# Kernel optimization log

Measured on AMD Instinct MI355X. Metric: run time of the kernel, lower is better.

Reference implementation:

```python
import jax, jax.numpy as jnp
import numpy as np


def setup_inputs() -> dict:
    key = jax.random.key(0)
    ks = jax.random.split(key, 6)
    B, T, S, E, D = 8, 128, 512, 512, 512  # batch, trg_len, src_len, enc_dim, trg_dim
    W_SCALE = 0.03  # small init to keep tanh unsaturated
    return {
        "hidden": jax.random.normal(ks[0], (B, T, D), jnp.float32),
        "encoder_outputs": jax.random.normal(ks[1], (B, S, E), jnp.float32),
        "encoder_mask": jnp.ones((B, S), jnp.float32),
        "W_attn": jax.random.normal(ks[2], (D, E + D), jnp.float32) * W_SCALE,
        "b_attn": jnp.zeros((D,), jnp.float32),
        "W_v": jax.random.normal(ks[3], (1, D), jnp.float32) * W_SCALE,
        "b_v": jnp.zeros((1,), jnp.float32),
        "W_out": jax.random.normal(ks[4], (D, E + D), jnp.float32) * W_SCALE,
    }


def masked_softmax(x, m, axis=-1):
    # faithful to repo: x*m, stable exp, e*m, normalize with eps
    x = x * m
    e_x = jnp.exp(x - jnp.max(x, axis=axis, keepdims=True))
    e_x = e_x * m
    return e_x / (jnp.sum(e_x, axis=axis, keepdims=True) + 1e-6)


def reference(hidden, encoder_outputs, encoder_mask, W_attn, b_attn, W_v, b_v, W_out):
    B, T, D = hidden.shape
    S = encoder_outputs.shape[1]
    # concat order in get_energy is (hidden_i, encoder_outputs), so split W_attn
    W_h = W_attn[:, :D]   # (D_out, trg_dim)
    W_e = W_attn[:, D:]   # (D_out, enc_dim)
    # Linear(concat) == h@W_h^T + e@W_e^T + b; vectorized over all (t, s) pairs
    hp = jnp.einsum('btd,kd->btk', hidden, W_h)            # (B,T,K)
    ep = jnp.einsum('bse,ke->bsk', encoder_outputs, W_e)   # (B,S,K)
    feat = jnp.tanh(hp[:, :, None, :] + ep[:, None, :, :] + b_attn)  # (B,T,S,K)
    energies = jnp.einsum('btsk,k->bts', feat, W_v[0]) + b_v[0]      # (B,T,S)
    # forward: energies * mask, then masked softmax
    m = encoder_mask[:, None, :]  # (B,1,S)
    energies = energies * m
    attn_weights = masked_softmax(energies, m, axis=-1)    # (B,T,S)
    weighted_context = jnp.einsum('bts,bse->bte', attn_weights, encoder_outputs)
    h_cat = jnp.concatenate([weighted_context, hidden], axis=-1)  # (B,T,E+D)
    h_tilde = jnp.tanh(jnp.einsum('btc,dc->btd', h_cat, W_out))   # (B,T,D)
    return h_tilde, weighted_context, attn_weights
```

## Files before the change

### kernel.cpp

```cpp
#include <hip/hip_runtime.h>
#include <hip/hip_bf16.h>
#include <math.h>

typedef unsigned short u16;
typedef unsigned int u32;
typedef __bf16 bf16x8 __attribute__((ext_vector_type(8)));
typedef float f32x4 __attribute__((ext_vector_type(4)));

#define OUT_WC   524288LL
#define OUT_ATTN 1048576LL
#define C2 2.8853900817779268f
#define LOG2E 1.4426950408889634f
#define LAS 40
#define LAS2 72

__device__ inline u16 f2b(float f) {
    return (u16)((__float_as_uint(f) + 0x8000u) >> 16);
}
__device__ inline float b2f(u16 v) { return __uint_as_float(((u32)v) << 16); }
__device__ inline u32 pkcvt(float x, float y) {
    __hip_bfloat162 h = __float22bfloat162_rn(make_float2(x, y));
    return *(u32*)&h;
}
__device__ inline float tanh_fast(float x) {
    return 1.f - 2.f * __builtin_amdgcn_rcpf(__builtin_amdgcn_exp2f(C2 * x) + 1.f);
}

__global__ __launch_bounds__(256) void proj(
    const float* __restrict__ hidden, const float* __restrict__ enc,
    const float* __restrict__ Wattn, const float* __restrict__ battn,
    const float* __restrict__ Wout,
    float* __restrict__ hp, u16* __restrict__ ept, float* __restrict__ hh,
    u16* __restrict__ enc_bf)
{
    __shared__ u16 lA[64 * LAS2];
    __shared__ u16 lB[64 * LAS2];
    const int tid = threadIdx.x;
    const int wvi = tid >> 6, ln = tid & 63;
    const int wm = wvi >> 1, wn = wvi & 1;
    const int l16 = ln & 15, quad = ln >> 4;
    const int blk = blockIdx.x;
    int bx, by, zz = 0, lda, ldb, mode;
    const float *A, *B;
    if (blk < 512) {
        mode = 0;
        zz = blk >> 6; by = (blk >> 3) & 7; bx = blk & 7;
        A = Wattn + 512; lda = 1024;
        B = enc + (long long)zz * 262144; ldb = 512;
    } else if (blk < 640) {
        mode = 1;
        int i = blk - 512; by = i >> 3; bx = i & 7;
        A = hidden; lda = 512;
        B = Wattn; ldb = 1024;
    } else {
        mode = 2;
        int i = blk - 640; by = i >> 3; bx = i & 7;
        A = hidden; lda = 512;
        B = Wout + 512; ldb = 1024;
    }
    const int m0 = by * 64, n0 = bx * 64;
    const int srow = tid >> 2, scol = (tid & 3) * 16;
    const float* Ap = A + (long long)(m0 + srow) * lda + scol;
    const float* Bp = B + (long long)(n0 + srow) * ldb + scol;
    const bool wr_enc = (mode == 0) && (by == 0);

    f32x4 acc00 = {0,0,0,0}, acc01 = {0,0,0,0}, acc10 = {0,0,0,0}, acc11 = {0,0,0,0};

    float4 pa0, pa1, pa2, pa3, pb0, pb1, pb2, pb3;
    #define PROJ_LOADK(k0) do { \
        pa0 = *(const float4*)(Ap + (k0));      pa1 = *(const float4*)(Ap + (k0) + 4);  \
        pa2 = *(const float4*)(Ap + (k0) + 8);  pa3 = *(const float4*)(Ap + (k0) + 12); \
        pb0 = *(const float4*)(Bp + (k0));      pb1 = *(const float4*)(Bp + (k0) + 4);  \
        pb2 = *(const float4*)(Bp + (k0) + 8);  pb3 = *(const float4*)(Bp + (k0) + 12); } while (0)

    PROJ_LOADK(0);
    for (int step = 0; step < 8; ++step) {
        uint4 av0 = make_uint4(pkcvt(pa0.x, pa0.y), pkcvt(pa0.z, pa0.w),
                               pkcvt(pa1.x, pa1.y), pkcvt(pa1.z, pa1.w));
        uint4 av1 = make_uint4(pkcvt(pa2.x, pa2.y), pkcvt(pa2.z, pa2.w),
                               pkcvt(pa3.x, pa3.y), pkcvt(pa3.z, pa3.w));
        uint4 bv0 = make_uint4(pkcvt(pb0.x, pb0.y), pkcvt(pb0.z, pb0.w),
                               pkcvt(pb1.x, pb1.y), pkcvt(pb1.z, pb1.w));
        uint4 bv1 = make_uint4(pkcvt(pb2.x, pb2.y), pkcvt(pb2.z, pb2.w),
                               pkcvt(pb3.x, pb3.y), pkcvt(pb3.z, pb3.w));
        if (wr_enc) {
            u16* ed = enc_bf + (long long)zz * 262144 +
                      (long long)(n0 + srow) * 512 + step * 64 + scol;
            *(uint4*)ed = bv0;
            *(uint4*)(ed + 8) = bv1;
        }
        __syncthreads();
        *(uint4*)&lA[srow * LAS2 + scol]     = av0;
        *(uint4*)&lA[srow * LAS2 + scol + 8] = av1;
        *(uint4*)&lB[srow * LAS2 + scol]     = bv0;
        *(uint4*)&lB[srow * LAS2 + scol + 8] = bv1;
        __syncthreads();
        if (step < 7) PROJ_LOADK((step + 1) * 64);
        #pragma unroll
        for (int kh = 0; kh < 2; ++kh) {
            bf16x8 a0 = *(const bf16x8*)&lA[(wm * 32      + l16) * LAS2 + kh * 32 + quad * 8];
            bf16x8 a1 = *(const bf16x8*)&lA[(wm * 32 + 16 + l16) * LAS2 + kh * 32 + quad * 8];
            bf16x8 b0 = *(const bf16x8*)&lB[(wn * 32      + l16) * LAS2 + kh * 32 + quad * 8];
            bf16x8 b1 = *(const bf16x8*)&lB[(wn * 32 + 16 + l16) * LAS2 + kh * 32 + quad * 8];
            acc00 = __builtin_amdgcn_mfma_f32_16x16x32_bf16(a0, b0, acc00, 0, 0, 0);
            acc01 = __builtin_amdgcn_mfma_f32_16x16x32_bf16(a0, b1, acc01, 0, 0, 0);
            acc10 = __builtin_amdgcn_mfma_f32_16x16x32_bf16(a1, b0, acc10, 0, 0, 0);
            acc11 = __builtin_amdgcn_mfma_f32_16x16x32_bf16(a1, b1, acc11, 0, 0, 0);
        }
    }
    #undef PROJ_LOADK

    const f32x4* accs[4] = { &acc00, &acc01, &acc10, &acc11 };
    #pragma unroll
    for (int i = 0; i < 2; ++i) {
        #pragma unroll
        for (int j = 0; j < 2; ++j) {
            const f32x4& a = *accs[i * 2 + j];
            #pragma unroll
            for (int r = 0; r < 4; ++r) {
                int m = m0 + wm * 32 + i * 16 + quad * 4 + r;
                int n = n0 + wn * 32 + j * 16 + l16;
                float v = a[r];
                if (mode == 0)
                    ept[(long long)zz * 262144 + (long long)m * 512 + n] =
                        f2b(__builtin_amdgcn_exp2f(C2 * v));
                else if (mode == 1)
                    hp[(long long)m * 512 + n] = C2 * (v + battn[n]);
                else
                    hh[(long long)m * 512 + n] = v;
            }
        }
    }
}

__device__ inline float wred_sum(float v) {
    #pragma unroll
    for (int i = 32; i > 0; i >>= 1) v += __shfl_xor(v, i);
    return v;
}
__device__ inline float wred_max(float v) {
    #pragma unroll
    for (int i = 32; i > 0; i >>= 1) v = fmaxf(v, __shfl_xor(v, i));
    return v;
}

__device__ inline void proc8(uint4 c, float4 hw, float* a0, float* a1) {
    u32 cc[4] = {c.x, c.y, c.z, c.w};
    #pragma unroll
    for (int i = 0; i < 4; ++i) {
        float xl = __uint_as_float(cc[i] << 16);
        float xh = __uint_as_float(cc[i] & 0xFFFF0000u);
        float rl0 = __builtin_amdgcn_rcpf(fmaf(hw.x, xl, 1.f));
        float rh0 = __builtin_amdgcn_rcpf(fmaf(hw.x, xh, 1.f));
        float rl1 = __builtin_amdgcn_rcpf(fmaf(hw.y, xl, 1.f));
        float rh1 = __builtin_amdgcn_rcpf(fmaf(hw.y, xh, 1.f));
        a0[2*i]   = fmaf(hw.z, rl0, a0[2*i]);
        a0[2*i+1] = fmaf(hw.z, rh0, a0[2*i+1]);
        a1[2*i]   = fmaf(hw.z, rl1, a1[2*i]);
        a1[2*i+1] = fmaf(hw.z, rh1, a1[2*i+1]);
    }
}
__device__ inline void wcproc2(uint4 c, float2 ap, float* acc0, float* acc1) {
    u32 cc[4] = {c.x, c.y, c.z, c.w};
    #pragma unroll
    for (int i = 0; i < 4; ++i) {
        float el = __uint_as_float(cc[i] << 16);
        float eh = __uint_as_float(cc[i] & 0xFFFF0000u);
        acc0[2*i]   = fmaf(ap.x, el, acc0[2*i]);
        acc0[2*i+1] = fmaf(ap.x, eh, acc0[2*i+1]);
        acc1[2*i]   = fmaf(ap.y, el, acc1[2*i]);
        acc1[2*i+1] = fmaf(ap.y, eh, acc1[2*i+1]);
    }
}

__global__ __launch_bounds__(1024) void energies(
    const float* __restrict__ maskp, const float* __restrict__ hp,
    const u16* __restrict__ ept, const float* __restrict__ Wv,
    const float* __restrict__ bvp, const u16* __restrict__ enc_bf,
    float* __restrict__ attn, float* __restrict__ wc)
{
    __shared__ __align__(16) float4 hpw[512];
    __shared__ float pa[2][16][512];
    __shared__ float aL[512][2];
    __shared__ float red[16];
    const int tid = threadIdx.x;
    const int b  = blockIdx.x & 7;
    const int t0 = (blockIdx.x >> 3) * 2;
    const int th = tid >> 9;
    const int k5 = tid & 511;
    const long long row0 = (long long)(b * 128 + t0) * 512;

    float hv = hp[row0 + (long long)th * 512 + k5];
    float eh = __builtin_amdgcn_exp2f(hv);
    float* hpwf = (float*)hpw;
    hpwf[k5 * 4 + th] = eh;
    float w = 0.f;
    if (th == 0) { w = Wv[k5]; hpwf[k5 * 4 + 2] = w; }
    float wsum = wred_sum(w);
    if ((tid & 63) == 0) red[tid >> 6] = wsum;
    __syncthreads();
    float sumWv = 0.f;
    #pragma unroll
    for (int i = 0; i < 16; ++i) sumWv += red[i];

    const int kg = tid >> 6, sl = tid & 63;
    const int s0 = sl * 8;
    const u16* eb = ept + (long long)b * 262144 + (kg * 32) * 512 + s0;
    const float4* hq = &hpw[kg * 32];

    float a0[8] = {0,0,0,0,0,0,0,0}, a1[8] = {0,0,0,0,0,0,0,0};
    uint4 c0 = *(const uint4*)(eb);
    uint4 c1 = *(const uint4*)(eb + 512);
    for (int kk = 0; kk < 30; kk += 2) {
        const u16* nb = eb + (kk + 2) * 512;
        uint4 n0 = *(const uint4*)(nb);
        uint4 n1 = *(const uint4*)(nb + 512);
        proc8(c0, hq[kk],     a0, a1);
        proc8(c1, hq[kk + 1], a0, a1);
        c0 = n0; c1 = n1;
    }
    proc8(c0, hq[30], a0, a1);
    proc8(c1, hq[31], a0, a1);

    *(float4*)&pa[0][kg][s0]     = make_float4(a0[0], a0[1], a0[2], a0[3]);
    *(float4*)&pa[0][kg][s0 + 4] = make_float4(a0[4], a0[5], a0[6], a0[7]);
    *(float4*)&pa[1][kg][s0]     = make_float4(a1[0], a1[1], a1[2], a1[3]);
    *(float4*)&pa[1][kg][s0 + 4] = make_float4(a1[4], a1[5], a1[6], a1[7]);
    __syncthreads();

    float A = 0.f;
    #pragma unroll
    for (int g = 0; g < 16; ++g) A += pa[th][g][k5];
    float mv = maskp[(long long)b * 512 + k5];
    float bv0 = bvp[0];
    float r = (bv0 + sumWv - 2.f * A) * mv; r *= mv;

    float vmax = wred_max(r);
    if ((tid & 63) == 0) red[tid >> 6] = vmax;
    __syncthreads();
    float mx = red[th * 8];
    #pragma unroll
    for (int i = 1; i < 8; ++i) mx = fmaxf(mx, red[th * 8 + i]);

    float ex = __builtin_amdgcn_exp2f((r - mx) * LOG2E) * mv;
    float vsum = wred_sum(ex);
    __syncthreads();
    if ((tid & 63) == 0) red[tid >> 6] = vsum;
    __syncthreads();
    float sm = 0.f;
    #pragma unroll
    for (int i = 0; i < 8; ++i) sm += red[th * 8 + i];
    float at = ex * (1.f / (sm + 1e-6f));
    attn[row0 + (long long)th * 512 + k5] = at;
    aL[k5][th] = at;
    __syncthreads();

    const int eg = tid & 63, sg = tid >> 6;
    const u16* encb = enc_bf + (long long)b * 262144 + (long long)(sg * 32) * 512 + eg * 8;
    const float2* aq = (const float2*)&aL[sg * 32][0];
    float acc0[8] = {0,0,0,0,0,0,0,0}, acc1[8] = {0,0,0,0,0,0,0,0};
    uint4 e0 = *(const uint4*)(encb);
    uint4 e1 = *(const uint4*)(encb + 512);
    for (int j = 0; j < 30; j += 2) {
        uint4 f0 = *(const uint4*)(encb + (long long)(j + 2) * 512);
        uint4 f1 = *(const uint4*)(encb + (long long)(j + 3) * 512);
        wcproc2(e0, aq[j],     acc0, acc1);
        wcproc2(e1, aq[j + 1], acc0, acc1);
        e0 = f0; e1 = f1;
    }
    wcproc2(e0, aq[30], acc0, acc1);
    wcproc2(e1, aq[31], acc0, acc1);

    *(float4*)&pa[0][sg][eg * 8]     = make_float4(acc0[0], acc0[1], acc0[2], acc0[3]);
    *(float4*)&pa[0][sg][eg * 8 + 4] = make_float4(acc0[4], acc0[5], acc0[6], acc0[7]);
    *(float4*)&pa[1][sg][eg * 8]     = make_float4(acc1[0], acc1[1], acc1[2], acc1[3]);
    *(float4*)&pa[1][sg][eg * 8 + 4] = make_float4(acc1[4], acc1[5], acc1[6], acc1[7]);
    __syncthreads();

    float wcv = 0.f;
    #pragma unroll
    for (int g = 0; g < 16; ++g) wcv += pa[th][g][k5];
    wc[row0 + (long long)th * 512 + k5] = wcv;
}

__global__ __launch_bounds__(256) void hout_k(
    const float* __restrict__ wc, const float* __restrict__ Wout,
    float* __restrict__ out)
{
    __shared__ u16 lA[32 * LAS];
    __shared__ u16 lB[64 * LAS];
    const int tid = threadIdx.x;
    const int wvi = tid >> 6, ln = tid & 63;
    const int l16 = ln & 15, quad = ln >> 4;
    const int msub = wvi & 1, npair = wvi >> 1;
    const int m0 = blockIdx.y * 32, n0 = blockIdx.x * 64;
    const int rowA = tid >> 3, kofA = (tid & 7) * 4;
    const int rowB = tid >> 2, kofB = (tid & 3) * 8;
    const float* Apw = wc + (long long)(m0 + rowA) * 512 + kofA;
    const float* Bpw = Wout + (long long)(n0 + rowB) * 1024 + kofB;
    f32x4 acc0 = {0,0,0,0}, acc1 = {0,0,0,0};

    float4 av, bw0, bw1;
    av  = *(const float4*)(Apw);
    bw0 = *(const float4*)(Bpw);
    bw1 = *(const float4*)(Bpw + 4);
    for (int k0 = 0; k0 < 512; k0 += 32) {
        uint2 aw = make_uint2(pkcvt(av.x, av.y), pkcvt(av.z, av.w));
        uint4 bv = make_uint4(pkcvt(bw0.x, bw0.y), pkcvt(bw0.z, bw0.w),
                              pkcvt(bw1.x, bw1.y), pkcvt(bw1.z, bw1.w));
        __syncthreads();
        *(uint2*)&lA[rowA * LAS + kofA] = aw;
        int kk = kofB ^ (((rowB >> 3) & 3) << 3);
        *(uint4*)&lB[rowB * LAS + kk] = bv;
        __syncthreads();
        if (k0 < 480) {
            av  = *(const float4*)(Apw + k0 + 32);
            bw0 = *(const float4*)(Bpw + k0 + 32);
            bw1 = *(const float4*)(Bpw + k0 + 36);
        }
        bf16x8 a = *(const bf16x8*)&lA[(msub * 16 + l16) * LAS + quad * 8];
        int nr0 = npair * 32 + l16, nr1 = nr0 + 16;
        bf16x8 b0 = *(const bf16x8*)&lB[nr0 * LAS + (quad * 8 ^ (((nr0 >> 3) & 3) << 3))];
        bf16x8 b1 = *(const bf16x8*)&lB[nr1 * LAS + (quad * 8 ^ (((nr1 >> 3) & 3) << 3))];
        acc0 = __builtin_amdgcn_mfma_f32_16x16x32_bf16(a, b0, acc0, 0, 0, 0);
        acc1 = __builtin_amdgcn_mfma_f32_16x16x32_bf16(a, b1, acc1, 0, 0, 0);
    }
    #pragma unroll
    for (int j = 0; j < 2; ++j) {
        const f32x4& a = j ? acc1 : acc0;
        #pragma unroll
        for (int r = 0; r < 4; ++r) {
            int m = m0 + msub * 16 + quad * 4 + r;
            int n = n0 + npair * 32 + j * 16 + l16;
            long long idx = (long long)m * 512 + n;
            out[idx] = tanh_fast(a[r] + out[idx]);
        }
    }
}

extern "C" void kernel_launch(void* const* d_in, const int* in_sizes, int n_in,
                              void* d_out, int out_size, void* d_ws, size_t ws_size,
                              hipStream_t stream)
{
    const float* hidden = (const float*)d_in[0];
    const float* enc    = (const float*)d_in[1];
    const float* mask   = (const float*)d_in[2];
    const float* Wattn  = (const float*)d_in[3];
    const float* battn  = (const float*)d_in[4];
    const float* Wv     = (const float*)d_in[5];
    const float* bvp    = (const float*)d_in[6];
    const float* Wout   = (const float*)d_in[7];
    float* out = (float*)d_out;

    float* hp     = (float*)d_ws;
    u16*   ept    = (u16*)((char*)d_ws + (2 << 20));
    u16*   enc_bf = (u16*)((char*)d_ws + (6 << 20));

    proj<<<768, 256, 0, stream>>>(hidden, enc, Wattn, battn, Wout,
                                  hp, ept, out , enc_bf);
    energies<<<512, 1024, 0, stream>>>(mask, hp, ept, Wv, bvp, enc_bf,
                                       out + OUT_ATTN, out + OUT_WC);
    hout_k<<<dim3(8, 32, 1), 256, 0, stream>>>(out + OUT_WC, Wout, out);
}
```

Baseline: 150.8 us.

## Fuse three kernels into one cooperative persistent kernel with grid syncs

Replaces the three separate launches (projection GEMMs, energies/softmax/context, output GEMM) with one cooperative kernel of 256 blocks of 1024 threads. Stages are separated by grid.sync. GEMM work is redistributed as 64x64 tasks handled by 16 waves, each computing one 16x16 tile, and each block processes two query-row pairs in the attention stage. This removes launch gaps and inter-kernel drains, at the cost of grid-wide barriers, lower occupancy (one block per CU), smaller per-wave MFMA work, and only half the blocks active in the final GEMM. It falls back to the old three-kernel path if the cooperative launch fails.

Result: slower. 501.1 us (+232.2%).

```diff
diff --git a/kernel.cpp b/kernel.cpp
--- a/kernel.cpp
+++ b/kernel.cpp
@@ -1,6 +1,9 @@
 #include <hip/hip_runtime.h>
 #include <hip/hip_bf16.h>
+#include <hip/hip_cooperative_groups.h>
 #include <math.h>
+
+namespace cg = cooperative_groups;
 
 typedef unsigned short u16;
 typedef unsigned int u32;
@@ -17,13 +20,50 @@
 __device__ inline u16 f2b(float f) {
     return (u16)((__float_as_uint(f) + 0x8000u) >> 16);
 }
-__device__ inline float b2f(u16 v) { return __uint_as_float(((u32)v) << 16); }
 __device__ inline u32 pkcvt(float x, float y) {
     __hip_bfloat162 h = __float22bfloat162_rn(make_float2(x, y));
     return *(u32*)&h;
 }
 __device__ inline float tanh_fast(float x) {
     return 1.f - 2.f * __builtin_amdgcn_rcpf(__builtin_amdgcn_exp2f(C2 * x) + 1.f);
+}
+__device__ inline float wred_sum(float v) {
+    #pragma unroll
+    for (int i = 32; i > 0; i >>= 1) v += __shfl_xor(v, i);
+    return v;
+}
+__device__ inline float wred_max(float v) {
+    #pragma unroll
+    for (int i = 32; i > 0; i >>= 1) v = fmaxf(v, __shfl_xor(v, i));
+    return v;
+}
+__device__ inline void proc8(uint4 c, float4 hw, float* a0, float* a1) {
+    u32 cc[4] = {c.x, c.y, c.z, c.w};
+    #pragma unroll
+    for (int i = 0; i < 4; ++i) {
+        float xl = __uint_as_float(cc[i] << 16);
+        float xh = __uint_as_float(cc[i] & 0xFFFF0000u);
+        float rl0 = __builtin_amdgcn_rcpf(fmaf(hw.x, xl, 1.f));
+        float rh0 = __builtin_amdgcn_rcpf(fmaf(hw.x, xh, 1.f));
+        float rl1 = __builtin_amdgcn_rcpf(fmaf(hw.y, xl, 1.f));
+        float rh1 = __builtin_amdgcn_rcpf(fmaf(hw.y, xh, 1.f));
+        a0[2*i]   = fmaf(hw.z, rl0, a0[2*i]);
+        a0[2*i+1] = fmaf(hw.z, rh0, a0[2*i+1]);
+        a1[2*i]   = fmaf(hw.z, rl1, a1[2*i]);
+        a1[2*i+1] = fmaf(hw.z, rh1, a1[2*i+1]);
+    }
+}
+__device__ inline void wcproc2(uint4 c, float2 ap, float* q0, float* q1) {
+    u32 cc[4] = {c.x, c.y, c.z, c.w};
+    #pragma unroll
+    for (int i = 0; i < 4; ++i) {
+        float el = __uint_as_float(cc[i] << 16);
+        float eh = __uint_as_float(cc[i] & 0xFFFF0000u);
+        q0[2*i]   = fmaf(ap.x, el, q0[2*i]);
+        q0[2*i+1] = fmaf(ap.x, eh, q0[2*i+1]);
+        q1[2*i]   = fmaf(ap.y, el, q1[2*i]);
+        q1[2*i+1] = fmaf(ap.y, eh, q1[2*i+1]);
+    }
 }
 
 __global__ __launch_bounds__(256) void proj(
@@ -43,20 +83,15 @@
     int bx, by, zz = 0, lda, ldb, mode;
     const float *A, *B;
     if (blk < 512) {
-        mode = 0;
-        zz = blk >> 6; by = (blk >> 3) & 7; bx = blk & 7;
+        mode = 0; zz = blk >> 6; by = (blk >> 3) & 7; bx = blk & 7;
         A = Wattn + 512; lda = 1024;
         B = enc + (long long)zz * 262144; ldb = 512;
     } else if (blk < 640) {
-        mode = 1;
-        int i = blk - 512; by = i >> 3; bx = i & 7;
-        A = hidden; lda = 512;
-        B = Wattn; ldb = 1024;
+        mode = 1; int i = blk - 512; by = i >> 3; bx = i & 7;
+        A = hidden; lda = 512; B = Wattn; ldb = 1024;
     } else {
-        mode = 2;
-        int i = blk - 640; by = i >> 3; bx = i & 7;
-        A = hidden; lda = 512;
-        B = Wout + 512; ldb = 1024;
+        mode = 2; int i = blk - 640; by = i >> 3; bx = i & 7;
+        A = hidden; lda = 512; B = Wout + 512; ldb = 1024;
     }
     const int m0 = by * 64, n0 = bx * 64;
     const int srow = tid >> 2, scol = (tid & 3) * 16;
@@ -65,14 +100,12 @@
     const bool wr_enc = (mode == 0) && (by == 0);
 
     f32x4 acc00 = {0,0,0,0}, acc01 = {0,0,0,0}, acc10 = {0,0,0,0}, acc11 = {0,0,0,0};
-
     float4 pa0, pa1, pa2, pa3, pb0, pb1, pb2, pb3;
     #define PROJ_LOADK(k0) do { \
         pa0 = *(const float4*)(Ap + (k0));      pa1 = *(const float4*)(Ap + (k0) + 4);  \
         pa2 = *(const float4*)(Ap + (k0) + 8);  pa3 = *(const float4*)(Ap + (k0) + 12); \
         pb0 = *(const float4*)(Bp + (k0));      pb1 = *(const float4*)(Bp + (k0) + 4);  \
         pb2 = *(const float4*)(Bp + (k0) + 8);  pb3 = *(const float4*)(Bp + (k0) + 12); } while (0)
-
     PROJ_LOADK(0);
     for (int step = 0; step < 8; ++step) {
         uint4 av0 = make_uint4(pkcvt(pa0.x, pa0.y), pkcvt(pa0.z, pa0.w),
@@ -109,7 +142,6 @@
         }
     }
     #undef PROJ_LOADK
-
     const f32x4* accs[4] = { &acc00, &acc01, &acc10, &acc11 };
     #pragma unroll
     for (int i = 0; i < 2; ++i) {
@@ -133,46 +165,6 @@
     }
 }
 
-__device__ inline float wred_sum(float v) {
-    #pragma unroll
-    for (int i = 32; i > 0; i >>= 1) v += __shfl_xor(v, i);
-    return v;
-}
-__device__ inline float wred_max(float v) {
-    #pragma unroll
-    for (int i = 32; i > 0; i >>= 1) v = fmaxf(v, __shfl_xor(v, i));
-    return v;
-}
-
-__device__ inline void proc8(uint4 c, float4 hw, float* a0, float* a1) {
-    u32 cc[4] = {c.x, c.y, c.z, c.w};
-    #pragma unroll
-    for (int i = 0; i < 4; ++i) {
-        float xl = __uint_as_float(cc[i] << 16);
-        float xh = __uint_as_float(cc[i] & 0xFFFF0000u);
-        float rl0 = __builtin_amdgcn_rcpf(fmaf(hw.x, xl, 1.f));
-        float rh0 = __builtin_amdgcn_rcpf(fmaf(hw.x, xh, 1.f));
-        float rl1 = __builtin_amdgcn_rcpf(fmaf(hw.y, xl, 1.f));
-        float rh1 = __builtin_amdgcn_rcpf(fmaf(hw.y, xh, 1.f));
-        a0[2*i]   = fmaf(hw.z, rl0, a0[2*i]);
-        a0[2*i+1] = fmaf(hw.z, rh0, a0[2*i+1]);
-        a1[2*i]   = fmaf(hw.z, rl1, a1[2*i]);
-        a1[2*i+1] = fmaf(hw.z, rh1, a1[2*i+1]);
-    }
-}
-__device__ inline void wcproc2(uint4 c, float2 ap, float* acc0, float* acc1) {
-    u32 cc[4] = {c.x, c.y, c.z, c.w};
-    #pragma unroll
-    for (int i = 0; i < 4; ++i) {
-        float el = __uint_as_float(cc[i] << 16);
-        float eh = __uint_as_float(cc[i] & 0xFFFF0000u);
-        acc0[2*i]   = fmaf(ap.x, el, acc0[2*i]);
-        acc0[2*i+1] = fmaf(ap.x, eh, acc0[2*i+1]);
-        acc1[2*i]   = fmaf(ap.y, el, acc1[2*i]);
-        acc1[2*i+1] = fmaf(ap.y, eh, acc1[2*i+1]);
-    }
-}
-
 __global__ __launch_bounds__(1024) void energies(
     const float* __restrict__ maskp, const float* __restrict__ hp,
     const u16* __restrict__ ept, const float* __restrict__ Wv,
@@ -258,23 +250,23 @@
     const int eg = tid & 63, sg = tid >> 6;
     const u16* encb = enc_bf + (long long)b * 262144 + (long long)(sg * 32) * 512 + eg * 8;
     const float2* aq = (const float2*)&aL[sg * 32][0];
-    float acc0[8] = {0,0,0,0,0,0,0,0}, acc1[8] = {0,0,0,0,0,0,0,0};
+    float q0[8] = {0,0,0,0,0,0,0,0}, q1[8] = {0,0,0,0,0,0,0,0};
     uint4 e0 = *(const uint4*)(encb);
     uint4 e1 = *(const uint4*)(encb + 512);
     for (int j = 0; j < 30; j += 2) {
         uint4 f0 = *(const uint4*)(encb + (long long)(j + 2) * 512);
         uint4 f1 = *(const uint4*)(encb + (long long)(j + 3) * 512);
-        wcproc2(e0, aq[j],     acc0, acc1);
-        wcproc2(e1, aq[j + 1], acc0, acc1);
+        wcproc2(e0, aq[j],     q0, q1);
+        wcproc2(e1, aq[j + 1], q0, q1);
         e0 = f0; e1 = f1;
     }
-    wcproc2(e0, aq[30], acc0, acc1);
-    wcproc2(e1, aq[31], acc0, acc1);
-
-    *(float4*)&pa[0][sg][eg * 8]     = make_float4(acc0[0], acc0[1], acc0[2], acc0[3]);
-    *(float4*)&pa[0][sg][eg * 8 + 4] = make_float4(acc0[4], acc0[5], acc0[6], acc0[7]);
-    *(float4*)&pa[1][sg][eg * 8]     = make_float4(acc1[0], acc1[1], acc1[2], acc1[3]);
-    *(float4*)&pa[1][sg][eg * 8 + 4] = make_float4(acc1[4], acc1[5], acc1[6], acc1[7]);
+    wcproc2(e0, aq[30], q0, q1);
+    wcproc2(e1, aq[31], q0, q1);
+
+    *(float4*)&pa[0][sg][eg * 8]     = make_float4(q0[0], q0[1], q0[2], q0[3]);
+    *(float4*)&pa[0][sg][eg * 8 + 4] = make_float4(q0[4], q0[5], q0[6], q0[7]);
+    *(float4*)&pa[1][sg][eg * 8]     = make_float4(q1[0], q1[1], q1[2], q1[3]);
+    *(float4*)&pa[1][sg][eg * 8 + 4] = make_float4(q1[4], q1[5], q1[6], q1[7]);
     __syncthreads();
 
     float wcv = 0.f;
@@ -338,6 +330,223 @@
     }
 }
 
+
+__device__ __forceinline__ void gemm_task(
+    int tsk, const float* __restrict__ hidden, const float* __restrict__ enc,
+    const float* __restrict__ Wattn, const float* __restrict__ battn,
+    const float* __restrict__ Wout, float* __restrict__ hp,
+    u16* __restrict__ ept, u16* __restrict__ enc_bf,
+    const float* __restrict__ wcp, float* __restrict__ outp,
+    u16* lA, u16* lB, int tid)
+{
+    int mode, bx, by, zz = 0, lda, ldb;
+    const float *A, *B;
+    if (tsk < 512) {
+        mode = 0; zz = tsk >> 6; by = (tsk >> 3) & 7; bx = tsk & 7;
+        A = Wattn + 512; lda = 1024;
+        B = enc + (long long)zz * 262144; ldb = 512;
+    } else if (tsk < 640) {
+        mode = 1; int i = tsk - 512; by = i >> 3; bx = i & 7;
+        A = hidden; lda = 512; B = Wattn; ldb = 1024;
+    } else if (tsk < 768) {
+        mode = 2; int i = tsk - 640; by = i >> 3; bx = i & 7;
+        A = hidden; lda = 512; B = Wout + 512; ldb = 1024;
+    } else {
+        mode = 3; int i = tsk - 768; by = i >> 3; bx = i & 7;
+        A = wcp; lda = 512; B = Wout; ldb = 1024;
+    }
+    const int m0 = by * 64, n0 = bx * 64;
+    const int srow = tid >> 4, sc = (tid & 15) * 4;
+    const int wvi = tid >> 6, ln = tid & 63;
+    const int wm = wvi >> 2, wn = wvi & 3;
+    const int l16 = ln & 15, quad = ln >> 4;
+    const float* Ap = A + (long long)(m0 + srow) * lda + sc;
+    const float* Bp = B + (long long)(n0 + srow) * ldb + sc;
+    const bool wr_enc = (mode == 0) && (by == 0);
+
+    f32x4 acc = {0,0,0,0};
+    float4 qa = *(const float4*)(Ap);
+    float4 qb = *(const float4*)(Bp);
+    for (int step = 0; step < 8; ++step) {
+        uint2 av = make_uint2(pkcvt(qa.x, qa.y), pkcvt(qa.z, qa.w));
+        uint2 bv = make_uint2(pkcvt(qb.x, qb.y), pkcvt(qb.z, qb.w));
+        if (wr_enc)
+            *(uint2*)(enc_bf + (long long)zz * 262144 +
+                      (long long)(n0 + srow) * 512 + step * 64 + sc) = bv;
+        __syncthreads();
+        *(uint2*)&lA[srow * LAS2 + sc] = av;
+        *(uint2*)&lB[srow * LAS2 + sc] = bv;
+        __syncthreads();
+        if (step < 7) {
+            qa = *(const float4*)(Ap + (step + 1) * 64);
+            qb = *(const float4*)(Bp + (step + 1) * 64);
+        }
+        #pragma unroll
+        for (int kh = 0; kh < 2; ++kh) {
+            bf16x8 a = *(const bf16x8*)&lA[(wm * 16 + l16) * LAS2 + kh * 32 + quad * 8];
+            bf16x8 b = *(const bf16x8*)&lB[(wn * 16 + l16) * LAS2 + kh * 32 + quad * 8];
+            acc = __builtin_amdgcn_mfma_f32_16x16x32_bf16(a, b, acc, 0, 0, 0);
+        }
+    }
+    #pragma unroll
+    for (int r = 0; r < 4; ++r) {
+        int m = m0 + wm * 16 + quad * 4 + r;
+        int n = n0 + wn * 16 + l16;
+        float v = acc[r];
+        long long idx = (long long)m * 512 + n;
+        if (mode == 0)
+            ept[(long long)zz * 262144 + idx] = f2b(__builtin_amdgcn_exp2f(C2 * v));
+        else if (mode == 1)
+            hp[idx] = C2 * (v + battn[n]);
+        else if (mode == 2)
+            outp[idx] = v;
+        else
+            outp[idx] = tanh_fast(v + outp[idx]);
+    }
+}
+
+__global__ __launch_bounds__(1024) void fused(
+    const float* __restrict__ hidden, const float* __restrict__ enc,
+    const float* __restrict__ maskp, const float* __restrict__ Wattn,
+    const float* __restrict__ battn, const float* __restrict__ Wv,
+    const float* __restrict__ bvp, const float* __restrict__ Wout,
+    float* __restrict__ out, float* __restrict__ hp,
+    u16* __restrict__ ept, u16* __restrict__ enc_bf)
+{
+    __shared__ __align__(16) char smem[77888];
+    u16* lA = (u16*)smem;
+    u16* lB = (u16*)(smem + 9216);
+    const int tid = threadIdx.x;
+    const int bid = blockIdx.x;
+    float* wcp   = out + OUT_WC;
+    float* attnp = out + OUT_ATTN;
+    cg::grid_group grid = cg::this_grid();
+
+    {
+        int t1 = ((bid & 7) << 6) | (bid >> 3);
+        gemm_task(t1,        hidden, enc, Wattn, battn, Wout, hp, ept, enc_bf, wcp, out, lA, lB, tid);
+        gemm_task(t1 + 32,   hidden, enc, Wattn, battn, Wout, hp, ept, enc_bf, wcp, out, lA, lB, tid);
+        gemm_task(512 + bid, hidden, enc, Wattn, battn, Wout, hp, ept, enc_bf, wcp, out, lA, lB, tid);
+    }
+    __threadfence();
+    grid.sync();
+    __threadfence();
+
+    {
+        float4* hpw = (float4*)smem;
+        float (*pa)[16][512] = (float (*)[16][512])(smem + 8192);
+        float (*aL)[2] = (float (*)[2])(smem + 73728);
+        float* red = (float*)(smem + 77824);
+        const int b = bid & 7;
+        const int th = tid >> 9, k5 = tid & 511;
+        const int kg = tid >> 6, sl = tid & 63;
+        const int s0 = sl * 8;
+        const float mv = maskp[(long long)b * 512 + k5];
+        const float bv0 = bvp[0];
+
+        for (int u = 0; u < 2; ++u) {
+            const int t0 = (((bid >> 3) << 1) | u) * 2;
+            const long long row0 = (long long)(b * 128 + t0) * 512;
+
+            float hv = hp[row0 + (long long)th * 512 + k5];
+            float ehv = __builtin_amdgcn_exp2f(hv);
+            float* hpwf = (float*)hpw;
+            hpwf[k5 * 4 + th] = ehv;
+            float w = 0.f;
+            if (th == 0) { w = Wv[k5]; hpwf[k5 * 4 + 2] = w; }
+            float wsum = wred_sum(w);
+            if ((tid & 63) == 0) red[tid >> 6] = wsum;
+            __syncthreads();
+            float sumWv = 0.f;
+            #pragma unroll
+            for (int i = 0; i < 16; ++i) sumWv += red[i];
+
+            const u16* eb = ept + (long long)b * 262144 + (kg * 32) * 512 + s0;
+            const float4* hq = &hpw[kg * 32];
+            float a0[8] = {0,0,0,0,0,0,0,0}, a1[8] = {0,0,0,0,0,0,0,0};
+            uint4 c0 = *(const uint4*)(eb);
+            uint4 c1 = *(const uint4*)(eb + 512);
+            for (int kk = 0; kk < 30; kk += 2) {
+                const u16* nb = eb + (kk + 2) * 512;
+                uint4 n0v = *(const uint4*)(nb);
+                uint4 n1v = *(const uint4*)(nb + 512);
+                proc8(c0, hq[kk],     a0, a1);
+                proc8(c1, hq[kk + 1], a0, a1);
+                c0 = n0v; c1 = n1v;
+            }
+            proc8(c0, hq[30], a0, a1);
+            proc8(c1, hq[31], a0, a1);
+
+            *(float4*)&pa[0][kg][s0]     = make_float4(a0[0], a0[1], a0[2], a0[3]);
+            *(float4*)&pa[0][kg][s0 + 4] = make_float4(a0[4], a0[5], a0[6], a0[7]);
+            *(float4*)&pa[1][kg][s0]     = make_float4(a1[0], a1[1], a1[2], a1[3]);
+            *(float4*)&pa[1][kg][s0 + 4] = make_float4(a1[4], a1[5], a1[6], a1[7]);
+            __syncthreads();
+
+            float A = 0.f;
+            #pragma unroll
+            for (int g = 0; g < 16; ++g) A += pa[th][g][k5];
+            float r = (bv0 + sumWv - 2.f * A) * mv; r *= mv;
+
+            float vmax = wred_max(r);
+            if ((tid & 63) == 0) red[tid >> 6] = vmax;
+            __syncthreads();
+            float mx = red[th * 8];
+            #pragma unroll
+            for (int i = 1; i < 8; ++i) mx = fmaxf(mx, red[th * 8 + i]);
+
+            float ex = __builtin_amdgcn_exp2f((r - mx) * LOG2E) * mv;
+            float vsum = wred_sum(ex);
+            __syncthreads();
+            if ((tid & 63) == 0) red[tid >> 6] = vsum;
+            __syncthreads();
+            float sm = 0.f;
+            #pragma unroll
+            for (int i = 0; i < 8; ++i) sm += red[th * 8 + i];
+            float at = ex * (1.f / (sm + 1e-6f));
+            attnp[row0 + (long long)th * 512 + k5] = at;
+            aL[k5][th] = at;
+            __syncthreads();
+
+            const int eg = tid & 63, sg = tid >> 6;
+            const u16* encb = enc_bf + (long long)b * 262144 +
+                              (long long)(sg * 32) * 512 + eg * 8;
+            const float2* aq = (const float2*)&aL[sg * 32][0];
+            float q0[8] = {0,0,0,0,0,0,0,0}, q1[8] = {0,0,0,0,0,0,0,0};
+            uint4 e0 = *(const uint4*)(encb);
+            uint4 e1 = *(const uint4*)(encb + 512);
+            for (int j = 0; j < 30; j += 2) {
+                uint4 f0 = *(const uint4*)(encb + (long long)(j + 2) * 512);
+                uint4 f1 = *(const uint4*)(encb + (long long)(j + 3) * 512);
+                wcproc2(e0, aq[j],     q0, q1);
+                wcproc2(e1, aq[j + 1], q0, q1);
+                e0 = f0; e1 = f1;
+            }
+            wcproc2(e0, aq[30], q0, q1);
+            wcproc2(e1, aq[31], q0, q1);
+
+            *(float4*)&pa[0][sg][eg * 8]     = make_float4(q0[0], q0[1], q0[2], q0[3]);
+            *(float4*)&pa[0][sg][eg * 8 + 4] = make_float4(q0[4], q0[5], q0[6], q0[7]);
+            *(float4*)&pa[1][sg][eg * 8]     = make_float4(q1[0], q1[1], q1[2], q1[3]);
+            *(float4*)&pa[1][sg][eg * 8 + 4] = make_float4(q1[4], q1[5], q1[6], q1[7]);
+            __syncthreads();
+
+            float wcv = 0.f;
+            #pragma unroll
+            for (int g = 0; g < 16; ++g) wcv += pa[th][g][k5];
+            wcp[row0 + (long long)th * 512 + k5] = wcv;
+            __syncthreads();
+        }
+    }
+    __threadfence();
+    grid.sync();
+    __threadfence();
+
+    if (bid < 128)
+        gemm_task(768 + bid, hidden, enc, Wattn, battn, Wout, hp, ept, enc_bf,
+                  wcp, out, lA, lB, tid);
+}
+
 extern "C" void kernel_launch(void* const* d_in, const int* in_sizes, int n_in,
                               void* d_out, int out_size, void* d_ws, size_t ws_size,
                               hipStream_t stream)
@@ -356,9 +565,17 @@
     u16*   ept    = (u16*)((char*)d_ws + (2 << 20));
     u16*   enc_bf = (u16*)((char*)d_ws + (6 << 20));
 
-    proj<<<768, 256, 0, stream>>>(hidden, enc, Wattn, battn, Wout,
-                                  hp, ept, out , enc_bf);
-    energies<<<512, 1024, 0, stream>>>(mask, hp, ept, Wv, bvp, enc_bf,
-                                       out + OUT_ATTN, out + OUT_WC);
-    hout_k<<<dim3(8, 32, 1), 256, 0, stream>>>(out + OUT_WC, Wout, out);
-}
+    void* kargs[] = { (void*)&hidden, (void*)&enc, (void*)&mask, (void*)&Wattn,
+                      (void*)&battn, (void*)&Wv, (void*)&bvp, (void*)&Wout,
+                      (void*)&out, (void*)&hp, (void*)&ept, (void*)&enc_bf };
+    hipError_t cerr = hipLaunchCooperativeKernel((const void*)fused, dim3(256),
+                                                 dim3(1024), kargs, 0, stream);
+    if (cerr != hipSuccess) {
+        (void)hipGetLastError();
+        proj<<<768, 256, 0, stream>>>(hidden, enc, Wattn, battn, Wout,
+                                      hp, ept, out , enc_bf);
+        energies<<<512, 1024, 0, stream>>>(mask, hp, ept, Wv, bvp, enc_bf,
+                                           out + OUT_ATTN, out + OUT_WC);
+        hout_k<<<dim3(8, 32, 1), 256, 0, stream>>>(out + OUT_WC, Wout, out);
+    }
+}
```
